# Optimization experiments

Measured on AMD Instinct MI355X. Metric: run time of the kernel, lower is better.

Reference implementation:

```python
import jax, jax.numpy as jnp
import numpy as np

NUM_TAGS = 32
START_ID = 29
STOP_ID = 30
PAD_ID = 31
VOCAB = 50000
EMB = 256
HID = 512          # bidirectional total; per-direction hidden = HID // 2
HD = HID // 2
B = 64
T = 512


def setup_inputs() -> dict:
    key = jax.random.key(0)
    ks = jax.random.split(key, 14)
    # pack_padded_sequence requires sorted-descending lengths; padding at the end
    lengths = np.sort(np.asarray(jax.random.randint(ks[0], (B,), T // 2, T + 1)))[::-1].copy()
    mask = (np.arange(T)[None, :] < lengths[:, None]).astype(np.int32)
    inp = jax.random.randint(ks[1], (B, T), 0, VOCAB, dtype=jnp.int32)
    gold = jax.random.randint(ks[2], (B, T), 0, START_ID, dtype=jnp.int32)  # real tags only
    s = 1.0 / np.sqrt(HD)
    emb = jax.random.normal(ks[3], (VOCAB, EMB), jnp.float32)
    Wih_f = jax.random.uniform(ks[4], (4 * HD, EMB), jnp.float32, -s, s)
    Whh_f = jax.random.uniform(ks[5], (4 * HD, HD), jnp.float32, -s, s)
    b_f = jax.random.uniform(ks[6], (4 * HD,), jnp.float32, -s, s)      # b_ih + b_hh combined
    Wih_b = jax.random.uniform(ks[7], (4 * HD, EMB), jnp.float32, -s, s)
    Whh_b = jax.random.uniform(ks[8], (4 * HD, HD), jnp.float32, -s, s)
    b_b = jax.random.uniform(ks[9], (4 * HD,), jnp.float32, -s, s)
    sl = 1.0 / np.sqrt(HID)
    W_tag = jax.random.uniform(ks[10], (NUM_TAGS, HID), jnp.float32, -sl, sl)
    b_tag = jax.random.uniform(ks[11], (NUM_TAGS,), jnp.float32, -sl, sl)
    trans = np.asarray(jax.random.normal(ks[12], (NUM_TAGS, NUM_TAGS), jnp.float32)).copy()
    # CRF.__init__ constraints
    trans[START_ID, :] = -10000.0
    trans[:, STOP_ID] = -10000.0
    trans[:, PAD_ID] = -10000.0
    trans[PAD_ID, :] = -10000.0
    trans[PAD_ID, STOP_ID] = 0.0
    trans[PAD_ID, PAD_ID] = 0.0
    return dict(inp=inp, gold=gold, mask=jnp.asarray(mask), emb=emb,
                Wih_f=Wih_f, Whh_f=Whh_f, b_f=b_f,
                Wih_b=Wih_b, Whh_b=Whh_b, b_b=b_b,
                W_tag=W_tag, b_tag=b_tag, trans=jnp.asarray(trans))


def _lstm_dir(xW, m, Whh):
    """xW: [T,B,4H] precomputed input projection + bias; m: [T,B,1] float mask; Whh: [4H,H].
    Masked state update replicates packed-sequence behavior (padding at sequence end)."""
    Bb, H = xW.shape[1], Whh.shape[1]

    def step(carry, xm):
        h, c = carry
        x_t, m_t = xm
        g = x_t + h @ Whh.T
        i, f, gg, o = jnp.split(g, 4, axis=-1)  # torch gate order i,f,g,o
        c_new = jax.nn.sigmoid(f) * c + jax.nn.sigmoid(i) * jnp.tanh(gg)
        h_new = jax.nn.sigmoid(o) * jnp.tanh(c_new)
        c = m_t * c_new + (1.0 - m_t) * c
        h = m_t * h_new + (1.0 - m_t) * h
        return (h, c), h

    init = (jnp.zeros((Bb, H), xW.dtype), jnp.zeros((Bb, H), xW.dtype))
    _, hs = jax.lax.scan(step, init, (xW, m))
    return hs  # [T,B,H]


def _forward(inp, gold, mask, emb, Wih_f, Whh_f, b_f, Wih_b, Whh_b, b_b, W_tag, b_tag, trans):
    maskf = mask.astype(jnp.float32)          # [B,T]
    x = emb[inp]                               # [B,T,E]
    xT = jnp.swapaxes(x, 0, 1)                 # [T,B,E]
    mT = maskf.T[:, :, None]                   # [T,B,1]
    h_f = _lstm_dir(xT @ Wih_f.T + b_f, mT, Whh_f)                 # forward direction
    h_b = _lstm_dir((xT @ Wih_b.T + b_b)[::-1], mT[::-1], Whh_b)[::-1]  # backward direction
    h = jnp.concatenate([h_f, h_b], axis=-1)   # [T,B,HID]
    h_tag = (h @ W_tag.T + b_tag) * mT         # masked emissions, [T,B,K]

    K = trans.shape[0]
    Bb = h_tag.shape[1]
    score0 = jnp.full((Bb, K), -10000.0, jnp.float32).at[:, STOP_ID].set(0.0)

    def crf_step(score, em):
        emit_t, m_t = em  # [B,K], [B,1]
        # logsumexp over previous tag j of score[b,j] + emit[b,i] + trans[i,j]
        s = jax.nn.logsumexp(score[:, None, :] + emit_t[:, :, None] + trans[None], axis=-1)
        return m_t * s + (1.0 - m_t) * score, None

    scoreZ, _ = jax.lax.scan(crf_step, score0, (h_tag, mT))
    Z = jax.nn.logsumexp(scoreZ + trans[STOP_ID], axis=-1)  # [B]

    # gold path score (vectorized version of CRF.score)
    h_bt = jnp.swapaxes(h_tag, 0, 1)                          # [B,T,K]
    emit = jnp.take_along_axis(h_bt[:, :-1, :], gold[:, 1:, None].astype(jnp.int32), axis=2)[..., 0]
    tr = trans[gold[:, 1:], gold[:, :-1]]                     # [B,T-1]
    gscore = jnp.sum((emit + tr) * maskf[:, :-1], axis=1)
    lengths = maskf.sum(1).astype(jnp.int32)
    last_tag = jnp.take_along_axis(gold, (lengths - 1)[:, None], axis=1)[:, 0]
    gscore = gscore + trans[STOP_ID, last_tag]
    return Z - gscore  # [B]


def reference(inp, gold, mask, emb, Wih_f, Whh_f, b_f, Wih_b, Whh_b, b_b, W_tag, b_tag, trans):
    return _forward(inp, gold, mask, emb, Wih_f, Whh_f, b_f, Wih_b, Whh_b, b_b, W_tag, b_tag, trans)
```

## Files before the change

kernel.cpp:

```cpp
#include <hip/hip_runtime.h>
#include <stdint.h>

#define T_LEN 512
#define NB 64
#define STOPID 30

typedef unsigned short u16;
typedef unsigned int u32;
typedef long long i64;
typedef short bf8 __attribute__((ext_vector_type(8)));
typedef float f32x4 __attribute__((ext_vector_type(4)));
typedef int v4i __attribute__((ext_vector_type(4)));

__device__ __forceinline__ float bf2f(u16 v){ return __uint_as_float(((u32)v) << 16); }
__device__ __forceinline__ u16 f2bf(float f){
  u32 u = __float_as_uint(f);
  return (u16)((u + 0x7FFFu + ((u >> 16) & 1u)) >> 16);
}
__device__ __forceinline__ float sigm(float x){
  return __builtin_amdgcn_rcpf(1.0f + __expf(-x));
}
__device__ __forceinline__ float tanhfast(float x){
  return 1.0f - 2.0f*__builtin_amdgcn_rcpf(1.0f + __expf(2.0f*x));
}
__device__ __forceinline__ v4i mk4(i64 a, i64 b){
  union { i64 q[2]; v4i v; } u; u.q[0]=a; u.q[1]=b; return u.v;
}

#define WSCALE 2032.0f
#define HSCALE 127.0f

extern "C" __global__ __launch_bounds__(256) void k0_cvt(
    const float* __restrict__ whf, const float* __restrict__ whb,
    const float* __restrict__ wif, const float* __restrict__ wib,
    const float* __restrict__ wtag,
    u32* __restrict__ whh8, u16* __restrict__ wih_bf, u16* __restrict__ wtag_bf)
{
  int i = blockIdx.x * 256 + threadIdx.x;
  wih_bf[i]          = f2bf(wif[i]);
  wih_bf[262144 + i] = f2bf(wib[i]);
  if (i < 16384) wtag_bf[i] = f2bf(wtag[i]);
  if (i < 131072) {
    const float* src = (i < 65536) ? (whf + (size_t)i*4) : (whb + (size_t)(i - 65536)*4);
    float4 v = *(const float4*)src;
    int b0 = (int)rintf(fminf(fmaxf(v.x*WSCALE, -127.f), 127.f));
    int b1 = (int)rintf(fminf(fmaxf(v.y*WSCALE, -127.f), 127.f));
    int b2 = (int)rintf(fminf(fmaxf(v.z*WSCALE, -127.f), 127.f));
    int b3 = (int)rintf(fminf(fmaxf(v.w*WSCALE, -127.f), 127.f));
    whh8[i] = (u32)(b0 & 0xFF) | ((u32)(b1 & 0xFF) << 8)
            | ((u32)(b2 & 0xFF) << 16) | ((u32)(b3 & 0xFF) << 24);
  }
}

extern "C" __global__ __launch_bounds__(256) void kg_emb(
    const int* __restrict__ inp, const float* __restrict__ emb,
    const int* __restrict__ mask, u16* __restrict__ xemb, int* __restrict__ lenv)
{
  int r = blockIdx.x*2 + (threadIdx.x >> 7);
  int col = (threadIdx.x & 127) * 2;
  int b = r & 63, t = r >> 6;
  int tok = inp[b*T_LEN + t];
  float2 v = *(const float2*)(emb + (size_t)tok*256 + col);
  u32 pk = ((u32)f2bf(v.x)) | (((u32)f2bf(v.y)) << 16);
  *(u32*)(xemb + (size_t)r*256 + col) = pk;
  if (blockIdx.x == 0 && threadIdx.x < 64) {
    const int* mrow = mask + threadIdx.x * T_LEN;
    int lo = 256, hi = 512;
    while (lo < hi) { int mid = (lo + hi) >> 1; if (mrow[mid]) lo = mid + 1; else hi = mid; }
    lenv[threadIdx.x] = lo;
  }
}

extern "C" __global__ __launch_bounds__(256, 1) void k1_proj(
    const u16* __restrict__ xemb, const u16* __restrict__ wih,
    const float* __restrict__ b_f, const float* __restrict__ b_b,
    u16* __restrict__ xW)
{
  int tc = blockIdx.x;
  int gb = blockIdx.y;
  int dir  = gb >> 4;
  int nblk = gb & 15;
  int w    = threadIdx.x >> 6;
  int lane = threadIdx.x & 63;
  int lr = lane & 15, q = lane >> 4;

  bf8 bw[4][8];
  const u16* wbase = wih + (size_t)dir*262144 + (size_t)nblk*64*256;
  #pragma unroll
  for (int n = 0; n < 4; ++n)
    #pragma unroll
    for (int kt = 0; kt < 8; ++kt)
      bw[n][kt] = *(const bf8*)(wbase + (size_t)(n*16 + lr)*256 + kt*32 + q*8);
  #pragma unroll
  for (int n = 0; n < 4; ++n) {
    asm volatile("" : "+a"(bw[n][0]), "+a"(bw[n][1]), "+a"(bw[n][2]), "+a"(bw[n][3]));
    asm volatile("" : "+a"(bw[n][4]), "+a"(bw[n][5]), "+a"(bw[n][6]), "+a"(bw[n][7]));
  }

  const float* bias = dir ? b_b : b_f;
  float4 bv[4];
  #pragma unroll
  for (int n = 0; n < 4; ++n) bv[n] = *(const float4*)(bias + nblk*64 + n*16 + q*4);

  for (int ti = 0; ti < 8; ++ti) {
    int t = tc*8 + ti;
    bf8 af[8];
    #pragma unroll
    for (int kt = 0; kt < 8; ++kt)
      af[kt] = *(const bf8*)(xemb + ((size_t)t*64 + w*16 + lr)*256 + kt*32 + q*8);

    f32x4 acc[4];
    #pragma unroll
    for (int n = 0; n < 4; ++n) { acc[n][0]=0.f; acc[n][1]=0.f; acc[n][2]=0.f; acc[n][3]=0.f; }
    #pragma unroll
    for (int kt = 0; kt < 8; ++kt)
      #pragma unroll
      for (int n = 0; n < 4; ++n)
        acc[n] = __builtin_amdgcn_mfma_f32_16x16x32_bf16(bw[n][kt], af[kt], acc[n], 0, 0, 0);

    u16* xp = xW + ((size_t)(dir*4 + w)*T_LEN + t)*16384 + (size_t)lr*1024;
    #pragma unroll
    for (int n = 0; n < 4; ++n) {
      ushort4 st;
      st.x = f2bf(acc[n][0] + bv[n].x);
      st.y = f2bf(acc[n][1] + bv[n].y);
      st.z = f2bf(acc[n][2] + bv[n].z);
      st.w = f2bf(acc[n][3] + bv[n].w);
      *(ushort4*)(xp + nblk*64 + n*16 + q*4) = st;
    }
  }
}

extern "C" __global__ __launch_bounds__(512, 2) void k2_lstm(
    const u32* __restrict__ whh8, const u16* __restrict__ xW,
    const int* __restrict__ lenv, u16* __restrict__ h_out)
{
  __shared__ __align__(16) unsigned char hb[2][16*264];
  __shared__ __align__(16) int rd[8][2][4][36];

  int blk = blockIdx.x;
  int dir  = blk >> 5;
  int rgrp = blk & 31;
  int r0   = rgrp * 2;
  int rg16 = rgrp >> 3;
  int rb2  = (rgrp & 7) * 2;
  int w   = threadIdx.x >> 6;
  int lane = threadIdx.x & 63;
  int lr = lane & 15, q = lane >> 4;
  int cw = w * 32;
  int row = lr & 1;
  int hi  = lr >> 1;
  int chb = q*8 + hi;

  for (int i = threadIdx.x; i < 1056; i += 512)
    ((unsigned long long*)hb)[i] = 0ull;

  v4i bw[4][2][4];
  const unsigned char* wb = (const unsigned char*)whh8 + (size_t)dir*262144;
  #pragma unroll
  for (int g = 0; g < 4; ++g)
    #pragma unroll
    for (int s2 = 0; s2 < 2; ++s2)
      #pragma unroll
      for (int kt = 0; kt < 4; ++kt)
        bw[g][s2][kt] = *(const v4i*)(wb + (size_t)(g*256 + cw + 16*s2 + lr)*256 + kt*64 + q*16);
  #pragma unroll
  for (int g = 0; g < 4; ++g)
    #pragma unroll
    for (int s2 = 0; s2 < 2; ++s2)
      asm volatile("" : "+a"(bw[g][s2][0]), "+a"(bw[g][s2][1]), "+a"(bw[g][s2][2]), "+a"(bw[g][s2][3]));

  float cst = 0.f, hst = 0.f;
  int lnr = lenv[r0 + row];
  int* rdw = &rd[w][0][0][0];
  const float ginv = 1.0f/(WSCALE*HSCALE);

  int t0 = dir ? (T_LEN-1) : 0;
  int tstep = dir ? -1 : 1;
  i64 xstep  = (i64)tstep * 16384;
  i64 hostep = (i64)tstep * (NB*256);

  const u16* xp = xW + (size_t)(dir*4 + rg16)*T_LEN*16384
                     + (size_t)(rb2 + row)*1024 + cw + chb + (size_t)t0*16384;
  u16* ho = h_out + ((size_t)(dir*T_LEN + t0)*NB + r0 + row)*256 + cw + chb;
  int tcur = t0;

  u16 xc[4];
  #pragma unroll
  for (int g = 0; g < 4; ++g) xc[g] = xp[g*256];

  v4i z4; z4[0]=0; z4[1]=0; z4[2]=0; z4[3]=0;
  asm volatile("" : "+v"(z4));
  __syncthreads();

  for (int s = 0; s < T_LEN; ++s) {
    const unsigned char* hr = hb[s & 1];
    v4i afv[4];
    #pragma unroll
    for (int kt = 0; kt < 4; ++kt) {
      i64 lo = *(const i64*)(hr + lr*264 + kt*64 + q*16);
      i64 hi8 = *(const i64*)(hr + lr*264 + kt*64 + q*16 + 8);
      afv[kt] = mk4(lo, hi8);
    }

    v4i acc[2][4];
    #pragma unroll
    for (int s2 = 0; s2 < 2; ++s2)
      #pragma unroll
      for (int g = 0; g < 4; ++g)
        acc[s2][g] = __builtin_amdgcn_mfma_i32_16x16x64_i8(bw[g][s2][0], afv[0], z4, 0, 0, 0);
    #pragma unroll
    for (int kt = 1; kt < 4; ++kt)
      #pragma unroll
      for (int s2 = 0; s2 < 2; ++s2)
        #pragma unroll
        for (int g = 0; g < 4; ++g)
          acc[s2][g] = __builtin_amdgcn_mfma_i32_16x16x64_i8(bw[g][s2][kt], afv[kt], acc[s2][g], 0, 0, 0);

    if (lr < 2) {
      #pragma unroll
      for (int s2 = 0; s2 < 2; ++s2)
        #pragma unroll
        for (int g = 0; g < 4; ++g)
          *(v4i*)&rdw[(lr*4 + g)*36 + s2*16 + q*4] = acc[s2][g];
    }

    u16 xn[4];
    xp += xstep;
    if (s < T_LEN-1) {
      #pragma unroll
      for (int g = 0; g < 4; ++g) xn[g] = xp[g*256];
    } else {
      #pragma unroll
      for (int g = 0; g < 4; ++g) xn[g] = xc[g];
    }

    float gv[4];
    #pragma unroll
    for (int g = 0; g < 4; ++g)
      gv[g] = (float)rdw[(row*4 + g)*36 + chb] * ginv + bf2f(xc[g]);

    bool mk = (tcur < lnr);
    float cn = sigm(gv[1])*cst + sigm(gv[0])*tanhfast(gv[2]);
    float hn = sigm(gv[3])*tanhfast(cn);
    cst = mk ? cn : cst;
    hst = mk ? hn : hst;

    *ho = f2bf(hst);
    ho += hostep;
    tcur += tstep;

    int q0 = (int)rintf(hst*HSCALE);
    unsigned char* hw = hb[(s+1) & 1];
    hw[row*264 + cw + chb] = (unsigned char)(q0 & 0xFF);

    #pragma unroll
    for (int g = 0; g < 4; ++g) xc[g] = xn[g];

    asm volatile("s_waitcnt lgkmcnt(0)\n\ts_barrier" ::: "memory");
  }
}

extern "C" __global__ __launch_bounds__(256, 2) void k3_emit(
    const u16* __restrict__ h_out, const u16* __restrict__ wtag_bf,
    const float* __restrict__ b_tag, float* __restrict__ em)
{
  int wv = threadIdx.x >> 6, lane = threadIdx.x & 63;
  int lr = lane & 15, q = lane >> 4;
  size_t r0 = ((size_t)blockIdx.x*4 + wv) * 16;

  bf8 a[16];
  #pragma unroll
  for (int kt = 0; kt < 16; ++kt) {
    const u16* hp = h_out + (size_t)(kt>>3)*T_LEN*NB*256 + (r0 + lr)*256 + (kt&7)*32 + q*8;
    a[kt] = *(const bf8*)hp;
  }
  f32x4 acc[2];
  acc[0][0]=0.f;acc[0][1]=0.f;acc[0][2]=0.f;acc[0][3]=0.f; acc[1]=acc[0];
  #pragma unroll
  for (int n = 0; n < 2; ++n) {
    #pragma unroll
    for (int kt = 0; kt < 16; ++kt) {
      bf8 bfr = *(const bf8*)(wtag_bf + (size_t)(n*16 + lr)*512 + kt*32 + q*8);
      acc[n] = __builtin_amdgcn_mfma_f32_16x16x32_bf16(a[kt], bfr, acc[n], 0, 0, 0);
    }
  }
  #pragma unroll
  for (int n = 0; n < 2; ++n) {
    float bt = b_tag[n*16 + lr];
    #pragma unroll
    for (int J = 0; J < 4; ++J)
      em[(r0 + q*4 + J)*32 + n*16 + lr] = acc[n][J] + bt;
  }
}

extern "C" __global__ __launch_bounds__(64) void k5_crf(
    const int* __restrict__ gold, const int* __restrict__ lenv,
    const float* __restrict__ em, const float* __restrict__ trans,
    float* __restrict__ out)
{
  __shared__ float trans_s[32][33];
  int tid = threadIdx.x;
  for (int i = tid; i < 1024; i += 64) trans_s[i>>5][i&31] = trans[i];
  __syncthreads();

  int j = tid & 31;
  int hf = tid >> 5;
  int p0 = hf * 16;
  int b = blockIdx.x;
  int len = lenv[b];
  float score = (j == STOPID) ? 0.f : -10000.f;
  float gscore = 0.f;
  int g_cur = gold[b*T_LEN];

  float tr16[16];
  #pragma unroll
  for (int pp = 0; pp < 16; ++pp) tr16[pp] = trans[j*32 + p0 + pp];

  float e = em[(size_t)b*32 + j];
  for (int t = 0; t < len; ++t) {
    float en = (t+1 < len) ? em[((size_t)(t+1)*64 + b)*32 + j] : 0.f;
    float sv[16];
    float m = -3.0e38f;
    #pragma unroll
    for (int pp = 0; pp < 16; ++pp) {
      float sp = __shfl(score, p0 + pp, 32);
      sv[pp] = sp + tr16[pp];
      m = fmaxf(m, sv[pp]);
    }
    m = fmaxf(m, __shfl_xor(m, 32));
    float se = 0.f;
    #pragma unroll
    for (int pp = 0; pp < 16; ++pp)
      se += __expf(sv[pp] - m);
    se += __shfl_xor(se, 32);
    score = e + m + __logf(se);
    if (t + 1 < T_LEN) {
      int g_next = gold[b*T_LEN + t + 1];
      float emg = __shfl(e, g_next, 32);
      gscore += emg + trans_s[g_next][g_cur];
      g_cur = g_next;
    }
    e = en;
  }
  float v = score + trans_s[STOPID][j];
  float m2 = v;
  #pragma unroll
  for (int off = 16; off; off >>= 1) m2 = fmaxf(m2, __shfl_xor(m2, off, 32));
  float se2 = __expf(v - m2);
  #pragma unroll
  for (int off = 16; off; off >>= 1) se2 += __shfl_xor(se2, off, 32);
  float Z = m2 + __logf(se2);
  if (tid == 0) {
    int g_last = gold[b*T_LEN + len - 1];
    out[b] = Z - (gscore + trans_s[STOPID][g_last]);
  }
}

extern "C" void kernel_launch(void* const* d_in, const int* in_sizes, int n_in,
                              void* d_out, int out_size, void* d_ws, size_t ws_size,
                              hipStream_t stream)
{
  const int*   inp   = (const int*)  d_in[0];
  const int*   gold  = (const int*)  d_in[1];
  const int*   mask  = (const int*)  d_in[2];
  const float* emb   = (const float*)d_in[3];
  const float* Wih_f = (const float*)d_in[4];
  const float* Whh_f = (const float*)d_in[5];
  const float* b_f   = (const float*)d_in[6];
  const float* Wih_b = (const float*)d_in[7];
  const float* Whh_b = (const float*)d_in[8];
  const float* b_b   = (const float*)d_in[9];
  const float* W_tag = (const float*)d_in[10];
  const float* b_tag = (const float*)d_in[11];
  const float* trans = (const float*)d_in[12];
  float* out = (float*)d_out;

  char* ws = (char*)d_ws;
  u32* whh8   = (u32*)(ws + 0);
  u16* wtag_bf= (u16*)(ws + 524288);
  u16* wih_bf = (u16*)(ws + 1048576);
  u16* xW     = (u16*)(ws + 2097152);
  float* em   = (float*)(ws + 2097152);
  u16* h_outp = (u16*)(ws + 136314880);
  u16* xemb   = (u16*)(ws + 136314880);
  int* lenv   = (int*)(ws + 169869312);

  hipLaunchKernelGGL(k0_cvt,  dim3(1024),     dim3(256), 0, stream,
                     Whh_f, Whh_b, Wih_f, Wih_b, W_tag, whh8, wih_bf, wtag_bf);
  hipLaunchKernelGGL(kg_emb,  dim3(16384),    dim3(256), 0, stream, inp, emb, mask, xemb, lenv);
  hipLaunchKernelGGL(k1_proj, dim3(64, 32),   dim3(256), 0, stream,
                     xemb, wih_bf, b_f, b_b, xW);
  hipLaunchKernelGGL(k2_lstm, dim3(64),       dim3(512), 0, stream,
                     whh8, xW, lenv, h_outp);
  hipLaunchKernelGGL(k3_emit, dim3(512),      dim3(256), 0, stream,
                     h_outp, wtag_bf, b_tag, em);
  hipLaunchKernelGGL(k5_crf,  dim3(64),       dim3(64),  0, stream,
                     gold, lenv, em, trans, out);
}
```

Measured before the change: 1.055 ms.

## Split LSTM recurrence to one batch row per block across 128 blocks

The recurrent LSTM kernel now runs one batch row per block with 4 waves of 256 threads over 128 blocks, instead of two rows per block with 8 waves over 64 blocks. Each wave keeps 64 output channels of int8 weights in AGPRs, which doubles the weight registers per thread. The hidden-state byte write into LDS is packed through lane shuffles into one 32-bit store per four lanes. The goal is more CUs working on the serial recurrence and a shorter per-step critical path, at the cost of more register pressure and more MFMA work per wave per step.

```diff
diff --git a/kernel.cpp b/kernel.cpp
--- a/kernel.cpp
+++ b/kernel.cpp
@@ -131,48 +131,44 @@
   }
 }
 
-extern "C" __global__ __launch_bounds__(512, 2) void k2_lstm(
+extern "C" __global__ __launch_bounds__(256, 1) void k2_lstm(
     const u32* __restrict__ whh8, const u16* __restrict__ xW,
     const int* __restrict__ lenv, u16* __restrict__ h_out)
 {
   __shared__ __align__(16) unsigned char hb[2][16*264];
-  __shared__ __align__(16) int rd[8][2][4][36];
+  __shared__ __align__(16) int rd[4][4][68];
 
   int blk = blockIdx.x;
-  int dir  = blk >> 5;
-  int rgrp = blk & 31;
-  int r0   = rgrp * 2;
-  int rg16 = rgrp >> 3;
-  int rb2  = (rgrp & 7) * 2;
-  int w   = threadIdx.x >> 6;
+  int dir = blk >> 6;
+  int r0  = blk & 63;
+  int rg16  = r0 >> 4;
+  int rowin = r0 & 15;
+  int w = threadIdx.x >> 6;
   int lane = threadIdx.x & 63;
   int lr = lane & 15, q = lane >> 4;
-  int cw = w * 32;
-  int row = lr & 1;
-  int hi  = lr >> 1;
-  int chb = q*8 + hi;
-
-  for (int i = threadIdx.x; i < 1056; i += 512)
+  int cw = w * 64;
+  int c  = threadIdx.x;
+
+  for (int i = threadIdx.x; i < 1056; i += 256)
     ((unsigned long long*)hb)[i] = 0ull;
 
-  v4i bw[4][2][4];
+  v4i bw[4][4][4];
   const unsigned char* wb = (const unsigned char*)whh8 + (size_t)dir*262144;
   #pragma unroll
   for (int g = 0; g < 4; ++g)
     #pragma unroll
-    for (int s2 = 0; s2 < 2; ++s2)
+    for (int m = 0; m < 4; ++m)
       #pragma unroll
       for (int kt = 0; kt < 4; ++kt)
-        bw[g][s2][kt] = *(const v4i*)(wb + (size_t)(g*256 + cw + 16*s2 + lr)*256 + kt*64 + q*16);
+        bw[g][m][kt] = *(const v4i*)(wb + (size_t)(g*256 + cw + m*16 + lr)*256 + kt*64 + q*16);
   #pragma unroll
   for (int g = 0; g < 4; ++g)
     #pragma unroll
-    for (int s2 = 0; s2 < 2; ++s2)
-      asm volatile("" : "+a"(bw[g][s2][0]), "+a"(bw[g][s2][1]), "+a"(bw[g][s2][2]), "+a"(bw[g][s2][3]));
+    for (int m = 0; m < 4; ++m)
+      asm volatile("" : "+a"(bw[g][m][0]), "+a"(bw[g][m][1]), "+a"(bw[g][m][2]), "+a"(bw[g][m][3]));
 
   float cst = 0.f, hst = 0.f;
-  int lnr = lenv[r0 + row];
-  int* rdw = &rd[w][0][0][0];
+  int lnr = lenv[r0];
   const float ginv = 1.0f/(WSCALE*HSCALE);
 
   int t0 = dir ? (T_LEN-1) : 0;
@@ -180,9 +176,8 @@
   i64 xstep  = (i64)tstep * 16384;
   i64 hostep = (i64)tstep * (NB*256);
 
-  const u16* xp = xW + (size_t)(dir*4 + rg16)*T_LEN*16384
-                     + (size_t)(rb2 + row)*1024 + cw + chb + (size_t)t0*16384;
-  u16* ho = h_out + ((size_t)(dir*T_LEN + t0)*NB + r0 + row)*256 + cw + chb;
+  const u16* xp = xW + ((size_t)(dir*4 + rg16)*T_LEN + t0)*16384 + (size_t)rowin*1024 + c;
+  u16* ho = h_out + ((size_t)(dir*T_LEN + t0)*NB + r0)*256 + c;
   int tcur = t0;
 
   u16 xc[4];
@@ -198,31 +193,31 @@
     v4i afv[4];
     #pragma unroll
     for (int kt = 0; kt < 4; ++kt) {
-      i64 lo = *(const i64*)(hr + lr*264 + kt*64 + q*16);
+      i64 lo  = *(const i64*)(hr + lr*264 + kt*64 + q*16);
       i64 hi8 = *(const i64*)(hr + lr*264 + kt*64 + q*16 + 8);
       afv[kt] = mk4(lo, hi8);
     }
 
-    v4i acc[2][4];
-    #pragma unroll
-    for (int s2 = 0; s2 < 2; ++s2)
+    v4i acc[4][4];
+    #pragma unroll
+    for (int g = 0; g < 4; ++g)
+      #pragma unroll
+      for (int m = 0; m < 4; ++m)
+        acc[g][m] = __builtin_amdgcn_mfma_i32_16x16x64_i8(bw[g][m][0], afv[0], z4, 0, 0, 0);
+    #pragma unroll
+    for (int kt = 1; kt < 4; ++kt)
       #pragma unroll
       for (int g = 0; g < 4; ++g)
-        acc[s2][g] = __builtin_amdgcn_mfma_i32_16x16x64_i8(bw[g][s2][0], afv[0], z4, 0, 0, 0);
-    #pragma unroll
-    for (int kt = 1; kt < 4; ++kt)
-      #pragma unroll
-      for (int s2 = 0; s2 < 2; ++s2)
         #pragma unroll
-        for (int g = 0; g < 4; ++g)
-          acc[s2][g] = __builtin_amdgcn_mfma_i32_16x16x64_i8(bw[g][s2][kt], afv[kt], acc[s2][g], 0, 0, 0);
-
-    if (lr < 2) {
-      #pragma unroll
-      for (int s2 = 0; s2 < 2; ++s2)
+        for (int m = 0; m < 4; ++m)
+          acc[g][m] = __builtin_amdgcn_mfma_i32_16x16x64_i8(bw[g][m][kt], afv[kt], acc[g][m], 0, 0, 0);
+
+    if (lr == 0) {
+      #pragma unroll
+      for (int g = 0; g < 4; ++g)
         #pragma unroll
-        for (int g = 0; g < 4; ++g)
-          *(v4i*)&rdw[(lr*4 + g)*36 + s2*16 + q*4] = acc[s2][g];
+        for (int m = 0; m < 4; ++m)
+          *(v4i*)&rd[w][g][m*16 + q*4] = acc[g][m];
     }
 
     u16 xn[4];
@@ -238,7 +233,7 @@
     float gv[4];
     #pragma unroll
     for (int g = 0; g < 4; ++g)
-      gv[g] = (float)rdw[(row*4 + g)*36 + chb] * ginv + bf2f(xc[g]);
+      gv[g] = (float)rd[w][g][lane] * ginv + bf2f(xc[g]);
 
     bool mk = (tcur < lnr);
     float cn = sigm(gv[1])*cst + sigm(gv[0])*tanhfast(gv[2]);
@@ -251,8 +246,12 @@
     tcur += tstep;
 
     int q0 = (int)rintf(hst*HSCALE);
+    u32 own = (u32)(q0 & 0xFF);
+    u32 v01 = own | (((u32)__shfl_xor((int)own, 1)) << 8);
+    u32 v03 = v01 | (((u32)__shfl_xor((int)v01, 2)) << 16);
     unsigned char* hw = hb[(s+1) & 1];
-    hw[row*264 + cw + chb] = (unsigned char)(q0 & 0xFF);
+    if ((lane & 3) == 0)
+      *(u32*)(hw + c) = v03;
 
     #pragma unroll
     for (int g = 0; g < 4; ++g) xc[g] = xn[g];
@@ -391,7 +390,7 @@
   hipLaunchKernelGGL(kg_emb,  dim3(16384),    dim3(256), 0, stream, inp, emb, mask, xemb, lenv);
   hipLaunchKernelGGL(k1_proj, dim3(64, 32),   dim3(256), 0, stream,
                      xemb, wih_bf, b_f, b_b, xW);
-  hipLaunchKernelGGL(k2_lstm, dim3(64),       dim3(512), 0, stream,
+  hipLaunchKernelGGL(k2_lstm, dim3(128),      dim3(256), 0, stream,
                      whh8, xW, lenv, h_outp);
   hipLaunchKernelGGL(k3_emit, dim3(512),      dim3(256), 0, stream,
                      h_outp, wtag_bf, b_tag, em);
```

After: 1.167 ms. 1.11x slower.
